# Kernel tuning notes

Measured on AMD Instinct MI355X. Metric: run time of the kernel, lower is better.

## Reference

```python
import jax, jax.numpy as jnp
import numpy as np
from math import sqrt, ceil

OUTPUT_DIM = 50257
INPUT_DIM = 1024
N_CLASSES = int(ceil(sqrt(OUTPUT_DIM)))            # 225
N_OUT_PER_CLASS = int(ceil(OUTPUT_DIM / N_CLASSES))  # 224


def setup_inputs() -> dict:
    key = jax.random.key(0)
    k_x, k_w1, k_w2 = jax.random.split(key, 3)
    X = jax.random.normal(k_x, (8, 128, INPUT_DIM), dtype=jnp.float32)
    # glorot-ish scale so softmax logits stay in a sane range
    s1 = float(np.sqrt(2.0 / (INPUT_DIM + N_CLASSES)))
    s2 = float(np.sqrt(2.0 / (INPUT_DIM + N_OUT_PER_CLASS)))
    W1 = jax.random.normal(k_w1, (INPUT_DIM, N_CLASSES), dtype=jnp.float32) * s1
    b1 = jnp.zeros((N_CLASSES,), dtype=jnp.float32)
    W2 = jax.random.normal(k_w2, (N_CLASSES, INPUT_DIM, N_OUT_PER_CLASS), dtype=jnp.float32) * s2
    b2 = jnp.zeros((N_CLASSES, N_OUT_PER_CLASS), dtype=jnp.float32)
    return {"X": X, "W1": W1, "b1": b1, "W2": W2, "b2": b2}


def reference(X, W1, b1, W2, b2):
    """Two-level hierarchical softmax, inference path (target=None).

    P(y) = softmax(x@W1+b1)[class(y)] * softmax(x@W2[class(y)]+b2[class(y)])[offset(y)]
    Computed densely over all classes and flattened to the full vocab.
    """
    B, L, D = X.shape
    x = X.reshape(-1, D)                                    # [N, D], N = B*L
    class_probs = jax.nn.softmax(x @ W1 + b1, axis=-1)      # [N, C]
    # per-class logits: [N, C, O]
    acts = jnp.einsum('nd,cdo->nco', x, W2) + b2
    within = jax.nn.softmax(acts, axis=-1)                  # [N, C, O]
    probs = within * class_probs[:, :, None]                # [N, C, O]
    probs = probs.reshape(x.shape[0], N_CLASSES * N_OUT_PER_CLASS)[:, :OUTPUT_DIM]
    return probs.reshape(B, L, OUTPUT_DIM)
```

## Files before the change

kernel.cpp:

```cpp
#include <hip/hip_runtime.h>
#include <hip/hip_bf16.h>

#define CLS 225
#define OPC 224
#define DIM 1024
#define NTOK 1024
#define VOCAB 50257

#define BM 128
#define BK 32
#define NT 14

typedef __attribute__((ext_vector_type(8))) short bf16x8;
typedef __attribute__((ext_vector_type(4))) float f32x4;

__device__ __forceinline__ unsigned short f2bf(float f) {
  unsigned u = __float_as_uint(f);
  u += 0x7FFFu + ((u >> 16) & 1u);
  return (unsigned short)(u >> 16);
}

__device__ __forceinline__ void gll16(const void* gsrc, void* ldst) {
  __builtin_amdgcn_global_load_lds(
      (const __attribute__((address_space(1))) void*)gsrc,
      (__attribute__((address_space(3))) void*)ldst, 16, 0, 0);
}

__global__ __launch_bounds__(256) void hs_cls_fused(
    const float* __restrict__ X, const float* __restrict__ W1,
    const float* __restrict__ b1, float* __restrict__ cls,
    unsigned short* __restrict__ Xws)
{
  const int r0 = blockIdx.x * 4;
  const int tid = threadIdx.x;

  __shared__ float xs[4][DIM];
  __shared__ float lg[4][CLS];

  {
    const float4* src = (const float4*)(X + (size_t)r0 * DIM);
    float4* dst = (float4*)xs;
    for (int i = tid; i < 4 * DIM / 4; i += 256) dst[i] = src[i];
  }
  __syncthreads();

  for (int i = tid; i < 512; i += 256) {
    const int r = i >> 7, grp = i & 127;
    const int t = grp >> 2, slot = grp & 3;
    const int n = r0 + r;
    const float* p = &xs[r][t * 32 + slot * 8];
    bf16x8 pk;
#pragma unroll
    for (int j = 0; j < 8; ++j) pk[j] = (short)f2bf(p[j]);
    const int wb = (n * 64 + slot * 16) ^ ((n & 7) << 4);
    *(bf16x8*)((char*)Xws + (size_t)t * 65536 + wb) = pk;
  }

  if (tid < CLS) {
    float acc0 = 0.f, acc1 = 0.f, acc2 = 0.f, acc3 = 0.f;
    const float* w1p = W1 + tid;
    for (int d = 0; d < DIM; d += 8) {
      float w[8];
#pragma unroll
      for (int u = 0; u < 8; ++u) w[u] = w1p[(size_t)(d + u) * CLS];
#pragma unroll
      for (int u = 0; u < 8; ++u) {
        acc0 += xs[0][d + u] * w[u];
        acc1 += xs[1][d + u] * w[u];
        acc2 += xs[2][d + u] * w[u];
        acc3 += xs[3][d + u] * w[u];
      }
    }
    const float bb = b1[tid];
    lg[0][tid] = acc0 + bb;
    lg[1][tid] = acc1 + bb;
    lg[2][tid] = acc2 + bb;
    lg[3][tid] = acc3 + bb;
  }
  __syncthreads();

  const int wave = tid >> 6, lane = tid & 63;
  {
    const int r = wave;
    float v[4];
    float m = -1e30f;
#pragma unroll
    for (int i = 0; i < 4; ++i) {
      const int c2 = lane + i * 64;
      v[i] = (c2 < CLS) ? lg[r][c2] : -1e30f;
      m = fmaxf(m, v[i]);
    }
#pragma unroll
    for (int mask = 32; mask >= 1; mask >>= 1) m = fmaxf(m, __shfl_xor(m, mask));
    float e[4];
    float s = 0.f;
#pragma unroll
    for (int i = 0; i < 4; ++i) {
      const int c2 = lane + i * 64;
      e[i] = (c2 < CLS) ? __expf(v[i] - m) : 0.f;
      s += e[i];
    }
#pragma unroll
    for (int mask = 32; mask >= 1; mask >>= 1) s += __shfl_xor(s, mask);
    const float inv = 1.f / s;
#pragma unroll
    for (int i = 0; i < 4; ++i) {
      const int c2 = lane + i * 64;
      if (c2 < CLS) cls[(size_t)(r0 + r) * CLS + c2] = e[i] * inv;
    }
  }
}

__global__ __launch_bounds__(256) void hs_cls_kernel(
    const float* __restrict__ X, const float* __restrict__ W1,
    const float* __restrict__ b1, float* __restrict__ cls)
{
  const int r0 = blockIdx.x * 4;
  const int tid = threadIdx.x;

  __shared__ float xs[4][DIM];
  __shared__ float lg[4][CLS];

  {
    const float4* src = (const float4*)(X + (size_t)r0 * DIM);
    float4* dst = (float4*)xs;
    for (int i = tid; i < 4 * DIM / 4; i += 256) dst[i] = src[i];
  }
  __syncthreads();

  if (tid < CLS) {
    float acc0 = 0.f, acc1 = 0.f, acc2 = 0.f, acc3 = 0.f;
    const float* w1p = W1 + tid;
    for (int d = 0; d < DIM; d += 8) {
      float w[8];
#pragma unroll
      for (int u = 0; u < 8; ++u) w[u] = w1p[(size_t)(d + u) * CLS];
#pragma unroll
      for (int u = 0; u < 8; ++u) {
        acc0 += xs[0][d + u] * w[u];
        acc1 += xs[1][d + u] * w[u];
        acc2 += xs[2][d + u] * w[u];
        acc3 += xs[3][d + u] * w[u];
      }
    }
    const float bb = b1[tid];
    lg[0][tid] = acc0 + bb;
    lg[1][tid] = acc1 + bb;
    lg[2][tid] = acc2 + bb;
    lg[3][tid] = acc3 + bb;
  }
  __syncthreads();

  const int wave = tid >> 6, lane = tid & 63;
  {
    const int r = wave;
    float v[4];
    float m = -1e30f;
#pragma unroll
    for (int i = 0; i < 4; ++i) {
      const int c2 = lane + i * 64;
      v[i] = (c2 < CLS) ? lg[r][c2] : -1e30f;
      m = fmaxf(m, v[i]);
    }
#pragma unroll
    for (int mask = 32; mask >= 1; mask >>= 1) m = fmaxf(m, __shfl_xor(m, mask));
    float e[4];
    float s = 0.f;
#pragma unroll
    for (int i = 0; i < 4; ++i) {
      const int c2 = lane + i * 64;
      e[i] = (c2 < CLS) ? __expf(v[i] - m) : 0.f;
      s += e[i];
    }
#pragma unroll
    for (int mask = 32; mask >= 1; mask >>= 1) s += __shfl_xor(s, mask);
    const float inv = 1.f / s;
#pragma unroll
    for (int i = 0; i < 4; ++i) {
      const int c2 = lane + i * 64;
      if (c2 < CLS) cls[(size_t)(r0 + r) * CLS + c2] = e[i] * inv;
    }
  }
}

__global__ __launch_bounds__(256) void w2_convert(
    const float* __restrict__ W2, unsigned short* __restrict__ W2ws)
{
  const int ct = blockIdx.x;
  const int c = ct >> 5, t = ct & 31;
  const float* src = W2 + ((size_t)c * DIM + (size_t)t * 32) * OPC;
  char* dst = (char*)(W2ws + (size_t)ct * (OPC * 32));
  for (int i = threadIdx.x; i < 896; i += 256) {
    const int o = i % OPC, slot = i / OPC;
    const float* p = src + (size_t)(slot * 8) * OPC + o;
    bf16x8 pk;
#pragma unroll
    for (int j = 0; j < 8; ++j) pk[j] = (short)f2bf(p[(size_t)j * OPC]);
    const int wb = (o * 64 + slot * 16) ^ ((o & 7) << 4);
    *(bf16x8*)(dst + wb) = pk;
  }
}

__global__ __launch_bounds__(256) void x_convert_linear(
    const float* __restrict__ X, unsigned short* __restrict__ Xbf)
{
  const int r0 = blockIdx.x * 16;
  for (int i = threadIdx.x; i < 16 * 128; i += 256) {
    const int r = i >> 7, grp = i & 127;
    const int n = r0 + r;
    const float* p = X + (size_t)n * DIM + grp * 8;
    bf16x8 pk;
#pragma unroll
    for (int j = 0; j < 8; ++j) pk[j] = (short)f2bf(p[j]);
    *(bf16x8*)(Xbf + (size_t)n * DIM + grp * 8) = pk;
  }
}

__global__ __launch_bounds__(256, 1) void hs_main2(
    const unsigned short* __restrict__ W2ws, const float* __restrict__ b2,
    const unsigned short* __restrict__ Xws, const float* __restrict__ cls,
    float* __restrict__ out)
{
  const int bid = blockIdx.x;
  const int g = bid >> 6;
  const int xcd = bid & 7;
  const int rt = (bid >> 3) & 7;
  const int c = g * 8 + xcd;
  if (c >= CLS) return;
  const int n0 = rt * BM;

  __shared__ __align__(16) char As[2][8192];
  __shared__ __align__(16) char Bs[2][16384];

  const int tid = threadIdx.x;
  const int wv = tid >> 6, lane = tid & 63;
  const int lo16 = lane & 15, hi4 = lane >> 4;
  const int loff = lane * 16;

  f32x4 acc[2][NT];
#pragma unroll
  for (int mt = 0; mt < 2; ++mt)
#pragma unroll
    for (int nt = 0; nt < NT; ++nt) acc[mt][nt] = (f32x4){0.f, 0.f, 0.f, 0.f};

  const char* xb  = (const char*)Xws + (size_t)n0 * 64 + loff;
  const char* wb2 = (const char*)W2ws + (size_t)c * 32 * 14336 + loff;
#define SEGDEF(i)                                                              \
  const int s_##i = wv * 6 + i;                                                \
  const bool isA_##i = (s_##i < 8);                                            \
  const char* g_##i = isA_##i ? (xb + s_##i * 1024) : (wb2 + (s_##i - 8) * 1024); \
  const size_t gstr_##i = isA_##i ? 65536u : 14336u;                           \
  const int ldo_##i = isA_##i ? s_##i * 1024 : (s_##i - 8) * 1024;
  SEGDEF(0) SEGDEF(1) SEGDEF(2) SEGDEF(3) SEGDEF(4) SEGDEF(5)

#define STG(i, buf, t)                                                         \
  gll16(g_##i + (size_t)(t) * gstr_##i, (isA_##i ? As[buf] : Bs[buf]) + ldo_##i)
#define STAGE(buf, t)                                                          \
  { STG(0, buf, t); STG(1, buf, t); STG(2, buf, t); STG(3, buf, t);            \
    STG(4, buf, t); STG(5, buf, t); }

#define COMPUTE(buf)                                                           \
  {                                                                            \
    const char* Ac = As[buf];                                                  \
    const char* Bc = Bs[buf];                                                  \
    const int ra = wv * 32 + lo16;                                             \
    const int axor = (lo16 & 7) << 4;                                          \
    const bf16x8 va0 = *(const bf16x8*)(Ac + ((ra * 64 + hi4 * 16) ^ axor));   \
    const bf16x8 va1 = *(const bf16x8*)(Ac + (((ra + 16) * 64 + hi4 * 16) ^ axor)); \
    _Pragma("unroll")                                                          \
    for (int nt = 0; nt < NT; ++nt) {                                          \
      const int o = nt * 16 + lo16;                                            \
      const bf16x8 vb = *(const bf16x8*)(Bc + ((o * 64 + hi4 * 16) ^ ((o & 7) << 4))); \
      acc[0][nt] = __builtin_amdgcn_mfma_f32_16x16x32_bf16(va0, vb, acc[0][nt], 0, 0, 0); \
      acc[1][nt] = __builtin_amdgcn_mfma_f32_16x16x32_bf16(va1, vb, acc[1][nt], 0, 0, 0); \
    }                                                                          \
  }

  STAGE(0, 0);
  STAGE(1, 1);

  for (int t = 0; t < 31; ++t) {
    asm volatile("s_waitcnt vmcnt(6)" ::: "memory");
    __builtin_amdgcn_s_barrier();
    __builtin_amdgcn_sched_barrier(0);

    COMPUTE(t & 1);

    __builtin_amdgcn_sched_barrier(0);
    __builtin_amdgcn_s_barrier();
    if (t < 30) STAGE(t & 1, t + 2);
  }
  asm volatile("s_waitcnt vmcnt(0)" ::: "memory");
  __builtin_amdgcn_s_barrier();
  __builtin_amdgcn_sched_barrier(0);
  COMPUTE(1);

#undef STAGE
#undef STG
#undef SEGDEF
#undef COMPUTE

  float b2v[NT];
#pragma unroll
  for (int nt = 0; nt < NT; ++nt) b2v[nt] = b2[c * OPC + nt * 16 + lo16];

#pragma unroll
  for (int mt = 0; mt < 2; ++mt) {
#pragma unroll
    for (int j = 0; j < 4; ++j) {
      const int n = n0 + wv * 32 + mt * 16 + hi4 * 4 + j;
      float vv[NT];
      float m = -1e30f;
#pragma unroll
      for (int nt = 0; nt < NT; ++nt) {
        vv[nt] = acc[mt][nt][j] + b2v[nt];
        m = fmaxf(m, vv[nt]);
      }
#pragma unroll
      for (int mask = 8; mask >= 1; mask >>= 1) m = fmaxf(m, __shfl_xor(m, mask));
      float s = 0.f;
#pragma unroll
      for (int nt = 0; nt < NT; ++nt) {
        vv[nt] = __expf(vv[nt] - m);
        s += vv[nt];
      }
#pragma unroll
      for (int mask = 8; mask >= 1; mask >>= 1) s += __shfl_xor(s, mask);
      const float scale = cls[(size_t)n * CLS + c] / s;
      const size_t rowbase = (size_t)n * VOCAB;
      const int colbase = c * OPC + lo16;
#pragma unroll
      for (int nt = 0; nt < NT; ++nt) {
        const int col = colbase + nt * 16;
        if (col < VOCAB)
          __builtin_nontemporal_store(vv[nt] * scale, out + rowbase + col);
      }
    }
  }
}

__global__ __launch_bounds__(256, 1) void hs_main_fallback(
    const float* __restrict__ W2, const float* __restrict__ b2,
    const unsigned short* __restrict__ Xbf, const float* __restrict__ cls,
    float* __restrict__ out)
{
  const int bid = blockIdx.x;
  const int g = bid >> 6;
  const int xcd = bid & 7;
  const int rt = (bid >> 3) & 7;
  const int c = g * 8 + xcd;
  if (c >= CLS) return;
  const int n0 = rt * BM;
  const float* __restrict__ W2c = W2 + (size_t)c * DIM * OPC;

  __shared__ __align__(16) char As[BM * BK * 2];
  __shared__ __align__(16) char Bs[OPC * BK * 2];

  const int tid = threadIdx.x;
  const int wv = tid >> 6, lane = tid & 63;
  const int lo16 = lane & 15, hi4 = lane >> 4;

  f32x4 acc[2][NT];
#pragma unroll
  for (int mt = 0; mt < 2; ++mt)
#pragma unroll
    for (int nt = 0; nt < NT; ++nt) acc[mt][nt] = (f32x4){0.f, 0.f, 0.f, 0.f};

  const int an0 = tid >> 2;
  const int akp = tid & 3;

  for (int k0 = 0; k0 < DIM; k0 += BK) {
    __syncthreads();
#pragma unroll
    for (int r = 0; r < 2; ++r) {
      const int n = an0 + r * 64;
      const uint4 raw = *(const uint4*)(Xbf + (size_t)(n0 + n) * DIM + k0 + akp * 8);
      const int wb = (n * 64 + akp * 16) ^ ((n & 7) << 4);
      *(uint4*)(As + wb) = raw;
    }
#pragma unroll
    for (int r = 0; r < 4; ++r) {
      const int t = tid + r * 256;
      if (t < 896) {
        const int o = t % OPC;
        const int kg = t / OPC;
        const float* p = W2c + (size_t)(k0 + kg * 8) * OPC + o;
        bf16x8 pk;
#pragma unroll
        for (int j = 0; j < 8; ++j) pk[j] = (short)f2bf(p[(size_t)j * OPC]);
        const int wb = (o * 64 + kg * 16) ^ ((o & 7) << 4);
        *(bf16x8*)(Bs + wb) = pk;
      }
    }
    __syncthreads();

    const int ra = wv * 32 + lo16;
    const int axor = (lo16 & 7) << 4;
    const bf16x8 a0 = *(const bf16x8*)(As + ((ra * 64 + hi4 * 16) ^ axor));
    const bf16x8 a1 = *(const bf16x8*)(As + (((ra + 16) * 64 + hi4 * 16) ^ axor));
#pragma unroll
    for (int nt = 0; nt < NT; ++nt) {
      const int o = nt * 16 + lo16;
      const bf16x8 b = *(const bf16x8*)(Bs + ((o * 64 + hi4 * 16) ^ ((o & 7) << 4)));
      acc[0][nt] = __builtin_amdgcn_mfma_f32_16x16x32_bf16(a0, b, acc[0][nt], 0, 0, 0);
      acc[1][nt] = __builtin_amdgcn_mfma_f32_16x16x32_bf16(a1, b, acc[1][nt], 0, 0, 0);
    }
  }

  float b2v[NT];
#pragma unroll
  for (int nt = 0; nt < NT; ++nt) b2v[nt] = b2[c * OPC + nt * 16 + lo16];

#pragma unroll
  for (int mt = 0; mt < 2; ++mt) {
#pragma unroll
    for (int j = 0; j < 4; ++j) {
      const int n = n0 + wv * 32 + mt * 16 + hi4 * 4 + j;
      float vv[NT];
      float m = -1e30f;
#pragma unroll
      for (int nt = 0; nt < NT; ++nt) {
        vv[nt] = acc[mt][nt][j] + b2v[nt];
        m = fmaxf(m, vv[nt]);
      }
#pragma unroll
      for (int mask = 8; mask >= 1; mask >>= 1) m = fmaxf(m, __shfl_xor(m, mask));
      float s = 0.f;
#pragma unroll
      for (int nt = 0; nt < NT; ++nt) {
        vv[nt] = __expf(vv[nt] - m);
        s += vv[nt];
      }
#pragma unroll
      for (int mask = 8; mask >= 1; mask >>= 1) s += __shfl_xor(s, mask);
      const float scale = cls[(size_t)n * CLS + c] / s;
      const size_t rowbase = (size_t)n * VOCAB;
      const int colbase = c * OPC + lo16;
#pragma unroll
      for (int nt = 0; nt < NT; ++nt) {
        const int col = colbase + nt * 16;
        if (col < VOCAB)
          __builtin_nontemporal_store(vv[nt] * scale, out + rowbase + col);
      }
    }
  }
}

extern "C" void kernel_launch(void* const* d_in, const int* in_sizes, int n_in,
                              void* d_out, int out_size, void* d_ws, size_t ws_size,
                              hipStream_t stream) {
  const float* X  = (const float*)d_in[0];
  const float* W1 = (const float*)d_in[1];
  const float* b1 = (const float*)d_in[2];
  const float* W2 = (const float*)d_in[3];
  const float* b2 = (const float*)d_in[4];
  float* out = (float*)d_out;

  const size_t W2WS = (size_t)CLS * DIM * OPC * 2;
  const size_t XWS  = (size_t)NTOK * DIM * 2;
  const size_t CLSZ = (size_t)NTOK * CLS * 4;

  if (ws_size >= W2WS + XWS + CLSZ) {
    unsigned short* W2ws = (unsigned short*)d_ws;
    unsigned short* Xws  = (unsigned short*)((char*)d_ws + W2WS);
    float* cls = (float*)((char*)d_ws + W2WS + XWS);

    w2_convert<<<CLS * 32, 256, 0, stream>>>(W2, W2ws);
    hs_cls_fused<<<NTOK / 4, 256, 0, stream>>>(X, W1, b1, cls, Xws);
    hs_main2<<<29 * 64, 256, 0, stream>>>(W2ws, b2, Xws, cls, out);
  } else {
    unsigned short* Xbf = (unsigned short*)d_ws;
    float* cls = (float*)((char*)d_ws + (size_t)NTOK * DIM * 2);

    x_convert_linear<<<NTOK / 16, 256, 0, stream>>>(X, Xbf);
    hs_cls_kernel<<<NTOK / 4, 256, 0, stream>>>(X, W1, b1, cls);
    hs_main_fallback<<<29 * 64, 256, 0, stream>>>(W2, b2, Xbf, cls, out);
  }
}
```

Before: 279.3 us.

## Split wave tile into 2x2 grid to cut B-fragment LDS reads

Each wave previously owned 32 rows by all 224 columns, re-reading every B fragment from LDS for only two MFMAs. Waves now form a 2x2 grid, each covering 64 rows by 112 columns, so every A and B fragment read feeds four MFMAs and per-step LDS traffic drops. Because each wave now sees only half of a class's columns, the row softmax needs a cross-wave merge of max and sum through a small shared buffer and an extra block barrier. The B swizzle now reuses the A xor term, which is only valid because o and lo16 share the same low three bits.

```diff
diff --git a/kernel.cpp b/kernel.cpp
--- a/kernel.cpp
+++ b/kernel.cpp
@@ -231,17 +231,19 @@
 
   __shared__ __align__(16) char As[2][8192];
   __shared__ __align__(16) char Bs[2][16384];
+  __shared__ float2 red[4][64];
 
   const int tid = threadIdx.x;
   const int wv = tid >> 6, lane = tid & 63;
   const int lo16 = lane & 15, hi4 = lane >> 4;
+  const int wr = wv >> 1, wc = wv & 1;
   const int loff = lane * 16;
 
-  f32x4 acc[2][NT];
-#pragma unroll
-  for (int mt = 0; mt < 2; ++mt)
-#pragma unroll
-    for (int nt = 0; nt < NT; ++nt) acc[mt][nt] = (f32x4){0.f, 0.f, 0.f, 0.f};
+  f32x4 acc[4][7];
+#pragma unroll
+  for (int m = 0; m < 4; ++m)
+#pragma unroll
+    for (int nt = 0; nt < 7; ++nt) acc[m][nt] = (f32x4){0.f, 0.f, 0.f, 0.f};
 
   const char* xb  = (const char*)Xws + (size_t)n0 * 64 + loff;
   const char* wb2 = (const char*)W2ws + (size_t)c * 32 * 14336 + loff;
@@ -263,16 +265,21 @@
   {                                                                            \
     const char* Ac = As[buf];                                                  \
     const char* Bc = Bs[buf];                                                  \
-    const int ra = wv * 32 + lo16;                                             \
     const int axor = (lo16 & 7) << 4;                                          \
-    const bf16x8 va0 = *(const bf16x8*)(Ac + ((ra * 64 + hi4 * 16) ^ axor));   \
-    const bf16x8 va1 = *(const bf16x8*)(Ac + (((ra + 16) * 64 + hi4 * 16) ^ axor)); \
+    bf16x8 Af[4];                                                              \
     _Pragma("unroll")                                                          \
-    for (int nt = 0; nt < NT; ++nt) {                                          \
-      const int o = nt * 16 + lo16;                                            \
-      const bf16x8 vb = *(const bf16x8*)(Bc + ((o * 64 + hi4 * 16) ^ ((o & 7) << 4))); \
-      acc[0][nt] = __builtin_amdgcn_mfma_f32_16x16x32_bf16(va0, vb, acc[0][nt], 0, 0, 0); \
-      acc[1][nt] = __builtin_amdgcn_mfma_f32_16x16x32_bf16(va1, vb, acc[1][nt], 0, 0, 0); \
+    for (int m = 0; m < 4; ++m) {                                              \
+      const int ra = wr * 64 + m * 16 + lo16;                                  \
+      Af[m] = *(const bf16x8*)(Ac + ((ra * 64 + hi4 * 16) ^ axor));            \
+    }                                                                          \
+    _Pragma("unroll")                                                          \
+    for (int nt = 0; nt < 7; ++nt) {                                           \
+      const int o = wc * 112 + nt * 16 + lo16;                                 \
+      const bf16x8 vb = *(const bf16x8*)(Bc + ((o * 64 + hi4 * 16) ^ axor));   \
+      _Pragma("unroll")                                                        \
+      for (int m = 0; m < 4; ++m)                                              \
+        acc[m][nt] = __builtin_amdgcn_mfma_f32_16x16x32_bf16(Af[m], vb,        \
+                                                             acc[m][nt], 0, 0, 0); \
     }                                                                          \
   }
 
@@ -300,40 +307,57 @@
 #undef SEGDEF
 #undef COMPUTE
 
-  float b2v[NT];
-#pragma unroll
-  for (int nt = 0; nt < NT; ++nt) b2v[nt] = b2[c * OPC + nt * 16 + lo16];
-
-#pragma unroll
-  for (int mt = 0; mt < 2; ++mt) {
+  float b2v[7];
+#pragma unroll
+  for (int nt = 0; nt < 7; ++nt) b2v[nt] = b2[c * OPC + wc * 112 + nt * 16 + lo16];
+
+  float pmx[4][4], psum[4][4];
+#pragma unroll
+  for (int m = 0; m < 4; ++m) {
 #pragma unroll
     for (int j = 0; j < 4; ++j) {
-      const int n = n0 + wv * 32 + mt * 16 + hi4 * 4 + j;
-      float vv[NT];
-      float m = -1e30f;
-#pragma unroll
-      for (int nt = 0; nt < NT; ++nt) {
-        vv[nt] = acc[mt][nt][j] + b2v[nt];
-        m = fmaxf(m, vv[nt]);
-      }
-#pragma unroll
-      for (int mask = 8; mask >= 1; mask >>= 1) m = fmaxf(m, __shfl_xor(m, mask));
+      float mx = -1e30f;
+#pragma unroll
+      for (int nt = 0; nt < 7; ++nt) {
+        acc[m][nt][j] += b2v[nt];
+        mx = fmaxf(mx, acc[m][nt][j]);
+      }
+#pragma unroll
+      for (int mask = 8; mask >= 1; mask >>= 1) mx = fmaxf(mx, __shfl_xor(mx, mask));
       float s = 0.f;
 #pragma unroll
-      for (int nt = 0; nt < NT; ++nt) {
-        vv[nt] = __expf(vv[nt] - m);
-        s += vv[nt];
+      for (int nt = 0; nt < 7; ++nt) {
+        const float v = __expf(acc[m][nt][j] - mx);
+        acc[m][nt][j] = v;
+        s += v;
       }
 #pragma unroll
       for (int mask = 8; mask >= 1; mask >>= 1) s += __shfl_xor(s, mask);
-      const float scale = cls[(size_t)n * CLS + c] / s;
+      pmx[m][j] = mx;
+      psum[m][j] = s;
+      if (lo16 == 0) red[wv][m * 16 + hi4 * 4 + j] = make_float2(mx, s);
+    }
+  }
+  __syncthreads();
+
+#pragma unroll
+  for (int m = 0; m < 4; ++m) {
+#pragma unroll
+    for (int j = 0; j < 4; ++j) {
+      const int rloc = m * 16 + hi4 * 4 + j;
+      const float2 ot = red[wv ^ 1][rloc];
+      const float mx = pmx[m][j], s = psum[m][j];
+      const float gm = fmaxf(mx, ot.x);
+      const float stot = s * __expf(mx - gm) + ot.y * __expf(ot.x - gm);
+      const int n = n0 + wr * 64 + rloc;
+      const float scale = cls[(size_t)n * CLS + c] * __expf(mx - gm) / stot;
       const size_t rowbase = (size_t)n * VOCAB;
-      const int colbase = c * OPC + lo16;
-#pragma unroll
-      for (int nt = 0; nt < NT; ++nt) {
+      const int colbase = c * OPC + wc * 112 + lo16;
+#pragma unroll
+      for (int nt = 0; nt < 7; ++nt) {
         const int col = colbase + nt * 16;
         if (col < VOCAB)
-          __builtin_nontemporal_store(vv[nt] * scale, out + rowbase + col);
+          __builtin_nontemporal_store(acc[m][nt][j] * scale, out + rowbase + col);
       }
     }
   }
```

Result: slower. 381.6 us (+36.6%).
